# Performance work log

Measured on AMD Instinct MI355X. Metric: run time of the kernel, lower is better.

Reference implementation:

```python
import jax, jax.numpy as jnp
import numpy as np

BETA = 0.95
THR = 1.0
SLOPE = 25.0


@jax.custom_vjp
def spike(x):
    # heaviside(x) with fast_sigmoid surrogate gradient (slope=25)
    return (x > 0).astype(x.dtype)

def _spike_fwd(x):
    return (x > 0).astype(x.dtype), x

def _spike_bwd(x, g):
    return (g / (SLOPE * jnp.abs(x) + 1.0) ** 2,)

spike.defvjp(_spike_fwd, _spike_bwd)


def setup_inputs() -> dict:
    key = jax.random.key(0)
    ks = jax.random.split(key, 16)
    T, B, D_in, H, C = 25, 128, 2048, 4096, 1000
    P_ACTIVE = 0.1

    def sparse_layer(kw, kb, km, fan_in, fan_out):
        bound = (6.0 / fan_in) ** 0.5  # kaiming_uniform with a=sqrt(5) -> U(-sqrt(6/fan_in)*?, ...); approx scale
        w = jax.random.uniform(kw, (fan_out, fan_in), minval=-bound, maxval=bound, dtype=jnp.float32)
        mask = (jax.random.uniform(km, (fan_out, fan_in)) < P_ACTIVE).astype(jnp.float32)
        # rescale rows by sqrt(fan_in / fan_in_active) on active weights
        fan_act = jnp.clip(mask.sum(axis=1, keepdims=True), 1.0, None)
        scale = jnp.where((fan_act > 0) & (fan_act < fan_in), (fan_in / fan_act) ** 0.5, 1.0)
        w = jnp.where(mask > 0, w * scale, w)
        fan_eff = jnp.maximum(mask.sum(axis=1).mean(), 1.0)
        b_bound = 1.0 / fan_eff ** 0.5
        b = jax.random.uniform(kb, (fan_out,), minval=-b_bound, maxval=b_bound, dtype=jnp.float32)
        return w, b, mask

    w1, b1, m1 = sparse_layer(ks[0], ks[1], ks[2], D_in, H)
    w2, b2, m2 = sparse_layer(ks[3], ks[4], ks[5], H, H)
    w3, b3, m3 = sparse_layer(ks[6], ks[7], ks[8], H, H)
    bo_bound = 1.0 / H ** 0.5
    w_out = jax.random.uniform(ks[9], (C, H), minval=-bo_bound, maxval=bo_bound, dtype=jnp.float32)
    b_out = jax.random.uniform(ks[10], (C,), minval=-bo_bound, maxval=bo_bound, dtype=jnp.float32)
    x_seq = jax.random.normal(ks[11], (T, B, D_in), dtype=jnp.float32)
    return {"x_seq": x_seq, "w1": w1, "b1": b1, "m1": m1, "w2": w2, "b2": b2, "m2": m2,
            "w3": w3, "b3": b3, "m3": m3, "w_out": w_out, "b_out": b_out}


def _lif(cur, mem):
    # snntorch Leaky, reset_mechanism='subtract': reset spike from PREVIOUS mem, detached
    reset = jax.lax.stop_gradient((mem > THR).astype(mem.dtype))
    mem_new = BETA * mem + cur - reset * THR
    spk = spike(mem_new - THR)
    return spk, mem_new


def reference(x_seq, w1, b1, m1, w2, b2, m2, w3, b3, m3, w_out, b_out):
    T, B, _ = x_seq.shape
    ew1 = w1 * m1  # effective weights cached once (math identical to per-step recompute)
    ew2 = w2 * m2
    ew3 = w3 * m3

    mem1 = jnp.zeros((B, ew1.shape[0]), x_seq.dtype)
    mem2 = jnp.zeros((B, ew2.shape[0]), x_seq.dtype)
    mem3 = jnp.zeros((B, ew3.shape[0]), x_seq.dtype)
    mem_o = jnp.zeros((B, w_out.shape[0]), x_seq.dtype)
    spk_sum = jnp.zeros((B, w_out.shape[0]), x_seq.dtype)

    def step(carry, x_t):
        mem1, mem2, mem3, mem_o, spk_sum = carry
        spk1, mem1 = _lif(x_t @ ew1.T + b1, mem1)
        spk2, mem2 = _lif(spk1 @ ew2.T + b2, mem2)
        spk3, mem3 = _lif(spk2 @ ew3.T + b3, mem3)
        spk_o, mem_o = _lif(spk3 @ w_out.T + b_out, mem_o)
        return (mem1, mem2, mem3, mem_o, spk_sum + spk_o), None

    (mem1, mem2, mem3, mem_o, spk_sum), _ = jax.lax.scan(
        step, (mem1, mem2, mem3, mem_o, spk_sum), x_seq)
    return spk_sum
```

## Files before the change

kernel.cpp:

```cpp
#include <hip/hip_runtime.h>

#define T_STEPS 25
#define BATCH   128
#define D_IN    2048
#define H_DIM   4096
#define C_DIM   1000
#define N_ALL   3200
#define GEMM_Q  320
#define P_K2048 7
#define P_K4096 13
#define WOT_LD  1024
#define BKA     16

typedef __attribute__((address_space(1))) const void gas_t;
typedef __attribute__((address_space(3))) void las_t;

__device__ __forceinline__ int panel_len(int rem) {
    return (rem >= 2 * GEMM_Q) ? GEMM_Q
         : (rem > GEMM_Q ? ((rem / 2 + 15) & ~15) : rem);
}

__global__ __launch_bounds__(256)
void tmask_k(float* __restrict__ dst, const float* __restrict__ src,
             const float* __restrict__ msk, int M, int K, int MT)
{
    __shared__ float t[32][33];
    const int tx = threadIdx.x, ty = threadIdx.y;
    const int k0 = blockIdx.x * 32, m0 = blockIdx.y * 32;
    #pragma unroll
    for (int i = 0; i < 4; ++i) {
        const int m = m0 + ty + 8 * i;
        float v = 0.f;
        if (m < M) {
            const size_t gi = (size_t)m * K + k0 + tx;
            v = src[gi];
            if (msk) v *= msk[gi];
        }
        t[ty + 8 * i][tx] = v;
    }
    __syncthreads();
    const int mc = m0 + tx;
    if (mc < MT) {
        #pragma unroll
        for (int i = 0; i < 4; ++i)
            dst[(size_t)(k0 + ty + 8 * i) * MT + mc] = t[tx][ty + 8 * i];
    }
}

#define FMAQ(AS, R)                                                   \
    acc[R].x = fmaf(AS, bv.x, acc[R].x);                              \
    acc[R].y = fmaf(AS, bv.y, acc[R].y);                              \
    acc[R].z = fmaf(AS, bv.z, acc[R].z);                              \
    acc[R].w = fmaf(AS, bv.w, acc[R].w);

__global__ __launch_bounds__(64)
void gemm_w(const float* __restrict__ AT, const float* __restrict__ B,
            float* __restrict__ part, int MT, int K, int ldb, int n0)
{
#pragma clang fp reassociate(off)
    __shared__ __align__(16) float As[2][BKA][16];
    const int lane = threadIdx.x;
    const int mg   = lane >> 5;
    const int lc   = lane & 31;
    const int m0   = blockIdx.y * 16;
    const int p    = blockIdx.x;

    int pstart = 0, rem = K, pl = panel_len(K);
    for (int i = 0; i < p; ++i) { pstart += pl; rem -= pl; pl = panel_len(rem); }
    const int nt = pl >> 4;

    float4 acc[8];
    #pragma unroll
    for (int r = 0; r < 8; ++r) acc[r] = make_float4(0.f, 0.f, 0.f, 0.f);

    const float* bp = B + (size_t)pstart * ldb + n0 + lc * 4;
    const int akr = lane >> 2, amq = (lane & 3) * 4;

    {
        const float* g = AT + (size_t)(pstart + akr) * MT + m0 + amq;
        __builtin_amdgcn_global_load_lds((gas_t*)g, (las_t*)&As[0][0][0], 16, 0, 0);
    }

    for (int ti = 0; ti < nt; ++ti) {
        const int k0 = pstart + (ti << 4);
        float4 bq[16];
        #pragma unroll
        for (int kk = 0; kk < BKA; ++kk)
            bq[kk] = *(const float4*)(bp + (size_t)kk * ldb);
        bp += (size_t)BKA * ldb;
        if (ti + 1 < nt) {
            const float* g = AT + (size_t)(k0 + BKA + akr) * MT + m0 + amq;
            __builtin_amdgcn_global_load_lds((gas_t*)g, (las_t*)&As[(ti + 1) & 1][0][0], 16, 0, 0);
            asm volatile("s_waitcnt vmcnt(1)" ::: "memory");
        } else {
            asm volatile("s_waitcnt vmcnt(0)" ::: "memory");
        }
        __builtin_amdgcn_sched_barrier(0);
        const int bf = ti & 1;
        #pragma unroll
        for (int kk = 0; kk < BKA; ++kk) {
            const float4 a0 = *(const float4*)&As[bf][kk][mg * 8];
            const float4 a1 = *(const float4*)&As[bf][kk][mg * 8 + 4];
            const float4 bv = bq[kk];
            FMAQ(a0.x, 0) FMAQ(a0.y, 1) FMAQ(a0.z, 2) FMAQ(a0.w, 3)
            FMAQ(a1.x, 4) FMAQ(a1.y, 5) FMAQ(a1.z, 6) FMAQ(a1.w, 7)
        }
    }

    const int mrow0 = m0 + mg * 8;
    #pragma unroll
    for (int r = 0; r < 8; ++r)
        *(float4*)&part[((size_t)p * MT + mrow0 + r) * BATCH + lc * 4] = acc[r];
}

__device__ __forceinline__ float lif1e(float c, float& m)
{
    const float r = (m > 1.0f) ? 1.0f : 0.0f;
    const float mn = __fsub_rn(__fadd_rn(__fmul_rn(0.95f, m), c), r);
    m = mn;
    return (mn > 1.0f) ? 1.0f : 0.0f;
}

__global__ __launch_bounds__(256)
void reduce_lif4(const float* __restrict__ part, int P, int Mdim,
                 const float* __restrict__ bias, float* __restrict__ mem,
                 float* __restrict__ spk)
{
#pragma clang fp reassociate(off)
    const int idx4 = blockIdx.x * 256 + threadIdx.x;
    const int idx = idx4 * 4;
    const size_t stride = (size_t)Mdim * BATCH;
    float4 tot = *(const float4*)&part[idx];
    for (int z = 1; z < P; ++z) {
        const float4 pv = *(const float4*)&part[(size_t)z * stride + idx];
        tot.x = __fadd_rn(tot.x, pv.x); tot.y = __fadd_rn(tot.y, pv.y);
        tot.z = __fadd_rn(tot.z, pv.z); tot.w = __fadd_rn(tot.w, pv.w);
    }
    const float bb = bias[idx >> 7];
    float4 mm = *(float4*)&mem[idx];
    float4 sp;
    sp.x = lif1e(__fadd_rn(tot.x, bb), mm.x);
    sp.y = lif1e(__fadd_rn(tot.y, bb), mm.y);
    sp.z = lif1e(__fadd_rn(tot.z, bb), mm.z);
    sp.w = lif1e(__fadd_rn(tot.w, bb), mm.w);
    *(float4*)&mem[idx] = mm;
    *(float4*)&spk[idx] = sp;
}

__global__ __launch_bounds__(256)
void reduce_lif_out4(const float* __restrict__ part, int P, int Mpad,
                     const float* __restrict__ bias, float* __restrict__ mem,
                     float* __restrict__ out)
{
#pragma clang fp reassociate(off)
    const int idx4 = blockIdx.x * 256 + threadIdx.x;
    if (idx4 >= (C_DIM * BATCH) / 4) return;
    const int idx = idx4 * 4;
    const int cc = idx >> 7, b = idx & 127;
    const size_t stride = (size_t)Mpad * BATCH;
    float4 tot = *(const float4*)&part[idx];
    for (int z = 1; z < P; ++z) {
        const float4 pv = *(const float4*)&part[(size_t)z * stride + idx];
        tot.x = __fadd_rn(tot.x, pv.x); tot.y = __fadd_rn(tot.y, pv.y);
        tot.z = __fadd_rn(tot.z, pv.z); tot.w = __fadd_rn(tot.w, pv.w);
    }
    const float bb = bias[cc];
    float4 mm = *(float4*)&mem[idx];
    float s;
    s = lif1e(__fadd_rn(tot.x, bb), mm.x); if (s > 0.f) out[(size_t)(b+0) * C_DIM + cc] += 1.0f;
    s = lif1e(__fadd_rn(tot.y, bb), mm.y); if (s > 0.f) out[(size_t)(b+1) * C_DIM + cc] += 1.0f;
    s = lif1e(__fadd_rn(tot.z, bb), mm.z); if (s > 0.f) out[(size_t)(b+2) * C_DIM + cc] += 1.0f;
    s = lif1e(__fadd_rn(tot.w, bb), mm.w); if (s > 0.f) out[(size_t)(b+3) * C_DIM + cc] += 1.0f;
    *(float4*)&mem[idx] = mm;
}

extern "C" void kernel_launch(void* const* d_in, const int* in_sizes, int n_in,
                              void* d_out, int out_size, void* d_ws, size_t ws_size,
                              hipStream_t stream)
{
    const float* x  = (const float*)d_in[0];
    const float* w1 = (const float*)d_in[1];
    const float* b1 = (const float*)d_in[2];
    const float* m1 = (const float*)d_in[3];
    const float* w2 = (const float*)d_in[4];
    const float* b2 = (const float*)d_in[5];
    const float* m2 = (const float*)d_in[6];
    const float* w3 = (const float*)d_in[7];
    const float* b3 = (const float*)d_in[8];
    const float* m3 = (const float*)d_in[9];
    const float* wo = (const float*)d_in[10];
    const float* bo = (const float*)d_in[11];
    float* out = (float*)d_out;
    float* ws  = (float*)d_ws;
    (void)in_sizes; (void)n_in; (void)ws_size;

    const size_t HB = (size_t)H_DIM * BATCH;
    const size_t CB = (size_t)C_DIM * BATCH;

    size_t off = 0;
    const size_t MEM1 = off; off += HB;
    const size_t MEM2 = off; off += HB;
    const size_t MEM3 = off; off += HB;
    const size_t MEMO = off; off += CB;
    const size_t stateFloats = off;
    const size_t SPK1 = off; off += HB;
    const size_t SPK2 = off; off += HB;
    const size_t SPK3 = off; off += HB;
    const size_t PART = off; off += (size_t)P_K4096 * HB;
    const size_t EWT1 = off; off += (size_t)D_IN * H_DIM;
    const size_t EWT2 = off; off += (size_t)H_DIM * H_DIM;
    const size_t EWT3 = off; off += (size_t)H_DIM * H_DIM;
    const size_t WOT  = off; off += (size_t)H_DIM * WOT_LD;
    const size_t XT   = off; off += (size_t)D_IN * N_ALL;

    hipMemsetAsync(d_ws, 0, stateFloats * sizeof(float), stream);
    hipMemsetAsync(d_out, 0, (size_t)out_size * sizeof(float), stream);

    {
        dim3 tb(32, 8);
        tmask_k<<<dim3(D_IN / 32, H_DIM / 32), tb, 0, stream>>>(ws + EWT1, w1, m1, H_DIM, D_IN, H_DIM);
        tmask_k<<<dim3(H_DIM / 32, H_DIM / 32), tb, 0, stream>>>(ws + EWT2, w2, m2, H_DIM, H_DIM, H_DIM);
        tmask_k<<<dim3(H_DIM / 32, H_DIM / 32), tb, 0, stream>>>(ws + EWT3, w3, m3, H_DIM, H_DIM, H_DIM);
        tmask_k<<<dim3(H_DIM / 32, WOT_LD / 32), tb, 0, stream>>>(ws + WOT, wo, nullptr, C_DIM, H_DIM, WOT_LD);
        tmask_k<<<dim3(D_IN / 32, N_ALL / 32), tb, 0, stream>>>(ws + XT, x, nullptr, N_ALL, D_IN, N_ALL);
    }

    const dim3 g1(P_K2048, H_DIM / 16);
    const dim3 g23(P_K4096, H_DIM / 16);
    const dim3 go(P_K4096, WOT_LD / 16);
    const int gLif4  = (int)(HB / 4 / 256);
    const int gLifO4 = (int)((CB / 4 + 255) / 256);

    for (int t = 0; t < T_STEPS; ++t) {
        gemm_w<<<g1, 64, 0, stream>>>(ws + EWT1, ws + XT, ws + PART,
                                      H_DIM, D_IN, N_ALL, t * BATCH);
        reduce_lif4<<<gLif4, 256, 0, stream>>>(ws + PART, P_K2048, H_DIM, b1, ws + MEM1, ws + SPK1);

        gemm_w<<<g23, 64, 0, stream>>>(ws + EWT2, ws + SPK1, ws + PART,
                                       H_DIM, H_DIM, BATCH, 0);
        reduce_lif4<<<gLif4, 256, 0, stream>>>(ws + PART, P_K4096, H_DIM, b2, ws + MEM2, ws + SPK2);

        gemm_w<<<g23, 64, 0, stream>>>(ws + EWT3, ws + SPK2, ws + PART,
                                       H_DIM, H_DIM, BATCH, 0);
        reduce_lif4<<<gLif4, 256, 0, stream>>>(ws + PART, P_K4096, H_DIM, b3, ws + MEM3, ws + SPK3);

        gemm_w<<<go, 64, 0, stream>>>(ws + WOT, ws + SPK3, ws + PART,
                                      WOT_LD, H_DIM, BATCH, 0);
        reduce_lif_out4<<<gLifO4, 256, 0, stream>>>(ws + PART, P_K4096, WOT_LD, bo, ws + MEMO, out);
    }
}
```

Before: 5.650 ms.

## Retile GEMM thread mapping and use 32-row tiles for hidden layers

Restructures the split-K GEMM so each lane computes RM rows by 8 batch columns instead of 8 rows by 4 columns, templated on RM. Hidden-layer GEMMs use 32-row tiles (RM=8) with a two-stage A load, which halves the number of blocks reading each B panel. B loads are split into two halves so the second half is fetched while the first is consumed. This aims to raise arithmetic intensity and reuse of B. In exchange it uses more accumulator registers and puts fewer blocks in flight for layers 2 and 3.

```diff
diff --git a/kernel.cpp b/kernel.cpp
--- a/kernel.cpp
+++ b/kernel.cpp
@@ -10,7 +10,6 @@
 #define P_K2048 7
 #define P_K4096 13
 #define WOT_LD  1024
-#define BKA     16
 
 typedef __attribute__((address_space(1))) const void gas_t;
 typedef __attribute__((address_space(3))) void las_t;
@@ -47,70 +46,119 @@
     }
 }
 
-#define FMAQ(AS, R)                                                   \
-    acc[R].x = fmaf(AS, bv.x, acc[R].x);                              \
-    acc[R].y = fmaf(AS, bv.y, acc[R].y);                              \
-    acc[R].z = fmaf(AS, bv.z, acc[R].z);                              \
-    acc[R].w = fmaf(AS, bv.w, acc[R].w);
-
+#define FMA8(AS, R)                                                   \
+    acc[R][0].x = fmaf(AS, bv0.x, acc[R][0].x);                       \
+    acc[R][0].y = fmaf(AS, bv0.y, acc[R][0].y);                       \
+    acc[R][0].z = fmaf(AS, bv0.z, acc[R][0].z);                       \
+    acc[R][0].w = fmaf(AS, bv0.w, acc[R][0].w);                       \
+    acc[R][1].x = fmaf(AS, bv1.x, acc[R][1].x);                       \
+    acc[R][1].y = fmaf(AS, bv1.y, acc[R][1].y);                       \
+    acc[R][1].z = fmaf(AS, bv1.z, acc[R][1].z);                       \
+    acc[R][1].w = fmaf(AS, bv1.w, acc[R][1].w);
+
+template<int RM>
 __global__ __launch_bounds__(64)
 void gemm_w(const float* __restrict__ AT, const float* __restrict__ B,
             float* __restrict__ part, int MT, int K, int ldb, int n0)
 {
 #pragma clang fp reassociate(off)
-    __shared__ __align__(16) float As[2][BKA][16];
+    constexpr int TM  = RM * 4;
+    constexpr int NST = (TM == 16) ? 1 : 2;
+    __shared__ __align__(16) float As[2][16][TM];
     const int lane = threadIdx.x;
-    const int mg   = lane >> 5;
-    const int lc   = lane & 31;
-    const int m0   = blockIdx.y * 16;
+    const int cg   = lane & 15;
+    const int mq   = lane >> 4;
+    const int m0   = blockIdx.y * TM;
     const int p    = blockIdx.x;
 
     int pstart = 0, rem = K, pl = panel_len(K);
     for (int i = 0; i < p; ++i) { pstart += pl; rem -= pl; pl = panel_len(rem); }
     const int nt = pl >> 4;
 
-    float4 acc[8];
+    float4 acc[RM][2];
     #pragma unroll
-    for (int r = 0; r < 8; ++r) acc[r] = make_float4(0.f, 0.f, 0.f, 0.f);
-
-    const float* bp = B + (size_t)pstart * ldb + n0 + lc * 4;
-    const int akr = lane >> 2, amq = (lane & 3) * 4;
+    for (int r = 0; r < RM; ++r) {
+        acc[r][0] = make_float4(0.f, 0.f, 0.f, 0.f);
+        acc[r][1] = make_float4(0.f, 0.f, 0.f, 0.f);
+    }
+
+    const float* bp = B + (size_t)pstart * ldb + n0 + cg * 8;
+    const int akr = (TM == 16) ? (lane >> 2) : (lane >> 3);
+    const int amq = (TM == 16) ? ((lane & 3) * 4) : ((lane & 7) * 4);
 
     {
         const float* g = AT + (size_t)(pstart + akr) * MT + m0 + amq;
         __builtin_amdgcn_global_load_lds((gas_t*)g, (las_t*)&As[0][0][0], 16, 0, 0);
+        if constexpr (NST == 2)
+            __builtin_amdgcn_global_load_lds((gas_t*)(g + 8 * (size_t)MT),
+                                             (las_t*)&As[0][8][0], 16, 0, 0);
     }
 
     for (int ti = 0; ti < nt; ++ti) {
         const int k0 = pstart + (ti << 4);
+        const int bf = ti & 1;
         float4 bq[16];
-        #pragma unroll
-        for (int kk = 0; kk < BKA; ++kk)
-            bq[kk] = *(const float4*)(bp + (size_t)kk * ldb);
-        bp += (size_t)BKA * ldb;
+
+        #pragma unroll
+        for (int kk = 0; kk < 8; ++kk) {
+            bq[2 * kk]     = *(const float4*)(bp + (size_t)kk * ldb);
+            bq[2 * kk + 1] = *(const float4*)(bp + (size_t)kk * ldb + 4);
+        }
         if (ti + 1 < nt) {
-            const float* g = AT + (size_t)(k0 + BKA + akr) * MT + m0 + amq;
-            __builtin_amdgcn_global_load_lds((gas_t*)g, (las_t*)&As[(ti + 1) & 1][0][0], 16, 0, 0);
-            asm volatile("s_waitcnt vmcnt(1)" ::: "memory");
+            const float* g = AT + (size_t)(k0 + 16 + akr) * MT + m0 + amq;
+            __builtin_amdgcn_global_load_lds((gas_t*)g, (las_t*)&As[bf ^ 1][0][0], 16, 0, 0);
+            if constexpr (NST == 2) {
+                __builtin_amdgcn_global_load_lds((gas_t*)(g + 8 * (size_t)MT),
+                                                 (las_t*)&As[bf ^ 1][8][0], 16, 0, 0);
+                asm volatile("s_waitcnt vmcnt(2)" ::: "memory");
+            } else {
+                asm volatile("s_waitcnt vmcnt(1)" ::: "memory");
+            }
         } else {
             asm volatile("s_waitcnt vmcnt(0)" ::: "memory");
         }
         __builtin_amdgcn_sched_barrier(0);
-        const int bf = ti & 1;
-        #pragma unroll
-        for (int kk = 0; kk < BKA; ++kk) {
-            const float4 a0 = *(const float4*)&As[bf][kk][mg * 8];
-            const float4 a1 = *(const float4*)&As[bf][kk][mg * 8 + 4];
-            const float4 bv = bq[kk];
-            FMAQ(a0.x, 0) FMAQ(a0.y, 1) FMAQ(a0.z, 2) FMAQ(a0.w, 3)
-            FMAQ(a1.x, 4) FMAQ(a1.y, 5) FMAQ(a1.z, 6) FMAQ(a1.w, 7)
-        }
-    }
-
-    const int mrow0 = m0 + mg * 8;
+        #pragma unroll
+        for (int kk = 0; kk < 8; ++kk) {
+            const float4 bv0 = bq[2 * kk], bv1 = bq[2 * kk + 1];
+            #pragma unroll
+            for (int r4 = 0; r4 < RM; r4 += 4) {
+                const float4 av = *(const float4*)&As[bf][kk][mq * RM + r4];
+                FMA8(av.x, r4 + 0)
+                FMA8(av.y, r4 + 1)
+                FMA8(av.z, r4 + 2)
+                FMA8(av.w, r4 + 3)
+            }
+        }
+
+        #pragma unroll
+        for (int kk = 0; kk < 8; ++kk) {
+            bq[2 * kk]     = *(const float4*)(bp + (size_t)(kk + 8) * ldb);
+            bq[2 * kk + 1] = *(const float4*)(bp + (size_t)(kk + 8) * ldb + 4);
+        }
+        bp += (size_t)16 * ldb;
+        asm volatile("s_waitcnt vmcnt(0)" ::: "memory");
+        __builtin_amdgcn_sched_barrier(0);
+        #pragma unroll
+        for (int kk = 8; kk < 16; ++kk) {
+            const float4 bv0 = bq[2 * (kk - 8)], bv1 = bq[2 * (kk - 8) + 1];
+            #pragma unroll
+            for (int r4 = 0; r4 < RM; r4 += 4) {
+                const float4 av = *(const float4*)&As[bf][kk][mq * RM + r4];
+                FMA8(av.x, r4 + 0)
+                FMA8(av.y, r4 + 1)
+                FMA8(av.z, r4 + 2)
+                FMA8(av.w, r4 + 3)
+            }
+        }
+    }
+
+    const int mrow0 = m0 + mq * RM;
     #pragma unroll
-    for (int r = 0; r < 8; ++r)
-        *(float4*)&part[((size_t)p * MT + mrow0 + r) * BATCH + lc * 4] = acc[r];
+    for (int r = 0; r < RM; ++r) {
+        *(float4*)&part[((size_t)p * MT + mrow0 + r) * BATCH + cg * 8]     = acc[r][0];
+        *(float4*)&part[((size_t)p * MT + mrow0 + r) * BATCH + cg * 8 + 4] = acc[r][1];
+    }
 }
 
 __device__ __forceinline__ float lif1e(float c, float& m)
@@ -226,26 +274,26 @@
     }
 
     const dim3 g1(P_K2048, H_DIM / 16);
-    const dim3 g23(P_K4096, H_DIM / 16);
+    const dim3 g23(P_K4096, H_DIM / 32);
     const dim3 go(P_K4096, WOT_LD / 16);
     const int gLif4  = (int)(HB / 4 / 256);
     const int gLifO4 = (int)((CB / 4 + 255) / 256);
 
     for (int t = 0; t < T_STEPS; ++t) {
-        gemm_w<<<g1, 64, 0, stream>>>(ws + EWT1, ws + XT, ws + PART,
-                                      H_DIM, D_IN, N_ALL, t * BATCH);
+        gemm_w<4><<<g1, 64, 0, stream>>>(ws + EWT1, ws + XT, ws + PART,
+                                         H_DIM, D_IN, N_ALL, t * BATCH);
         reduce_lif4<<<gLif4, 256, 0, stream>>>(ws + PART, P_K2048, H_DIM, b1, ws + MEM1, ws + SPK1);
 
-        gemm_w<<<g23, 64, 0, stream>>>(ws + EWT2, ws + SPK1, ws + PART,
-                                       H_DIM, H_DIM, BATCH, 0);
+        gemm_w<8><<<g23, 64, 0, stream>>>(ws + EWT2, ws + SPK1, ws + PART,
+                                          H_DIM, H_DIM, BATCH, 0);
         reduce_lif4<<<gLif4, 256, 0, stream>>>(ws + PART, P_K4096, H_DIM, b2, ws + MEM2, ws + SPK2);
 
-        gemm_w<<<g23, 64, 0, stream>>>(ws + EWT3, ws + SPK2, ws + PART,
-                                       H_DIM, H_DIM, BATCH, 0);
+        gemm_w<8><<<g23, 64, 0, stream>>>(ws + EWT3, ws + SPK2, ws + PART,
+                                          H_DIM, H_DIM, BATCH, 0);
         reduce_lif4<<<gLif4, 256, 0, stream>>>(ws + PART, P_K4096, H_DIM, b3, ws + MEM3, ws + SPK3);
 
-        gemm_w<<<go, 64, 0, stream>>>(ws + WOT, ws + SPK3, ws + PART,
-                                      WOT_LD, H_DIM, BATCH, 0);
+        gemm_w<4><<<go, 64, 0, stream>>>(ws + WOT, ws + SPK3, ws + PART,
+                                         WOT_LD, H_DIM, BATCH, 0);
         reduce_lif_out4<<<gLifO4, 256, 0, stream>>>(ws + PART, P_K4096, WOT_LD, bo, ws + MEMO, out);
     }
 }
```

Measured after the change: 5.594 ms. About the same (-1.0%).
